# Kernel tuning notes

Hardware: AMD Instinct MI355X
Metric: run time of the kernel (lower is better)

The kernel has to match this reference:

```python
import jax, jax.numpy as jnp
import numpy as np

D_MODEL = 1024
NUM_HEADS = 16
HEAD_DIM = D_MODEL // NUM_HEADS


def setup_inputs() -> dict:
    key = jax.random.key(0)
    ks = jax.random.split(key, 9)
    s = 1.0 / np.sqrt(D_MODEL)  # torch Linear default init range scale
    def lin(k):
        kw, kb = jax.random.split(k)
        W = jax.random.uniform(kw, (D_MODEL, D_MODEL), jnp.float32, -s, s)
        b = jax.random.uniform(kb, (D_MODEL,), jnp.float32, -s, s)
        return W, b
    Wq, bq = lin(ks[0])
    Wk, bk = lin(ks[1])
    Wv, bv = lin(ks[2])
    Wo, bo = lin(ks[3])
    x = jax.random.normal(ks[4], (4, 2048, D_MODEL), jnp.float32)
    return {"x": x, "Wq": Wq, "bq": bq, "Wk": Wk, "bk": bk,
            "Wv": Wv, "bv": bv, "Wo": Wo, "bo": bo}


def reference(x, Wq, bq, Wk, bk, Wv, bv, Wo, bo):
    B, S, _ = x.shape
    H, Dh = NUM_HEADS, HEAD_DIM
    scale = Dh ** -0.5
    # projections; W stored as [in, out] so y = x @ W + b
    q = (x @ Wq + bq).reshape(B, S, H, Dh).transpose(0, 2, 1, 3)  # [B,H,S,Dh]
    k = (x @ Wk + bk).reshape(B, S, H, Dh).transpose(0, 2, 1, 3)
    v = (x @ Wv + bv).reshape(B, S, H, Dh).transpose(0, 2, 1, 3)
    scores = jnp.einsum('bhqd,bhkd->bhqk', q, k) * scale  # [B,H,S,S]
    causal = jnp.tril(jnp.ones((S, S), dtype=bool))
    scores = jnp.where(causal[None, None], scores, jnp.finfo(scores.dtype).min)
    attn = jax.nn.softmax(scores, axis=-1)
    out = jnp.einsum('bhqk,bhkd->bhqd', attn, v)  # [B,H,S,Dh]
    out = out.transpose(0, 2, 1, 3).reshape(B, S, H * Dh)
    return out @ Wo + bo
```

## Files before the change

kernel.cpp:

```cpp
#include <hip/hip_runtime.h>
#include <math.h>

#define DM 1024
#define NH 16
#define DH 64
#define BB 4
#define SS 2048
#define MROWS (BB*SS)

typedef __bf16 bf16;
typedef __bf16 bf16x2 __attribute__((ext_vector_type(2)));
typedef __bf16 bf16x8 __attribute__((ext_vector_type(8)));
typedef float floatx4 __attribute__((ext_vector_type(4)));
typedef unsigned int uintx4 __attribute__((ext_vector_type(4)));
typedef unsigned int uintx2 __attribute__((ext_vector_type(2)));

#if __has_builtin(__builtin_amdgcn_exp2f)
#define EXP2F __builtin_amdgcn_exp2f
#else
#define EXP2F exp2f
#endif

#define QSCALE (0.125f * 1.44269504088896f)

__device__ __forceinline__ void cp16(void* lds, const void* g) {
  __builtin_amdgcn_global_load_lds(
      (__attribute__((address_space(1))) void*)(void*)g,
      (__attribute__((address_space(3))) void*)lds,
      16, 0, 0);
}

__device__ __forceinline__ unsigned pk2(float a, float b) {
  bf16x2 t;
  t[0] = (bf16)a;
  t[1] = (bf16)b;
  return __builtin_bit_cast(unsigned, t);
}

#if __has_builtin(__builtin_amdgcn_permlane32_swap) && \
    __has_builtin(__builtin_amdgcn_permlane16_swap)
__device__ __forceinline__ void pl32(unsigned& a, unsigned& b) {
  uintx2 r = __builtin_amdgcn_permlane32_swap(a, b, false, false);
  a = r[0]; b = r[1];
}
__device__ __forceinline__ void pl16(unsigned& a, unsigned& b) {
  uintx2 r = __builtin_amdgcn_permlane16_swap(a, b, false, false);
  a = r[0]; b = r[1];
}
#else
__device__ __forceinline__ void pl32(unsigned& a, unsigned& b) {
  asm volatile("v_permlane32_swap_b32 %0, %1" : "+v"(a), "+v"(b));
}
__device__ __forceinline__ void pl16(unsigned& a, unsigned& b) {
  asm volatile("v_permlane16_swap_b32 %0, %1" : "+v"(a), "+v"(b));
}
#endif

__global__ __launch_bounds__(256) void cvt_x(
    const float* __restrict__ X, bf16* __restrict__ Y) {
  int i = (blockIdx.x * 256 + threadIdx.x) * 8;
  float4 a = *(const float4*)&X[i];
  float4 b = *(const float4*)&X[i + 4];
  bf16x8 o;
  o[0] = (bf16)a.x; o[1] = (bf16)a.y; o[2] = (bf16)a.z; o[3] = (bf16)a.w;
  o[4] = (bf16)b.x; o[5] = (bf16)b.y; o[6] = (bf16)b.z; o[7] = (bf16)b.w;
  *(bf16x8*)&Y[i] = o;
}

__global__ __launch_bounds__(1024) void wtransc(
    const float* __restrict__ W0, const float* __restrict__ W1,
    const float* __restrict__ W2, const float* __restrict__ W3,
    bf16* __restrict__ T0, bf16* __restrict__ T1,
    bf16* __restrict__ T2, bf16* __restrict__ T3) {
  __shared__ float tile[32][33];
  const float* W; bf16* T;
  int z = blockIdx.z;
  if (z == 0)      { W = W0; T = T0; }
  else if (z == 1) { W = W1; T = T1; }
  else if (z == 2) { W = W2; T = T2; }
  else             { W = W3; T = T3; }
  int tx = threadIdx.x, ty = threadIdx.y;
  tile[ty][tx] = W[(blockIdx.y * 32 + ty) * DM + blockIdx.x * 32 + tx];
  __syncthreads();
  T[(blockIdx.x * 32 + ty) * DM + blockIdx.y * 32 + tx] = (bf16)tile[tx][ty];
}

#define BK 32
#define TST 136

__global__ __launch_bounds__(256, 3) void gemm_qkv(
    const bf16* __restrict__ A, const bf16* __restrict__ WT,
    const float* __restrict__ bq, const float* __restrict__ bk,
    const float* __restrict__ bv,
    bf16* __restrict__ qb, bf16* __restrict__ kb, bf16* __restrict__ vt) {
  __shared__ __align__(16) char smem[2 * 128 * BK * 2 * 2 > 128 * TST * 2
                                         ? 2 * 128 * BK * 2 * 2
                                         : 128 * TST * 2];
  bf16* As = (bf16*)smem;
  bf16* Bs = (bf16*)smem + 2 * 128 * BK;
  bf16* Ts = (bf16*)smem;

  int tid = threadIdx.x;
  int lane = tid & 63, w = tid >> 6;
  int wm = (w >> 1) * 64;
  int wn = (w & 1) * 64;
  int m0 = blockIdx.y * 128;
  int n0 = blockIdx.x * 128;
  int which = n0 >> 10;
  int qd = lane >> 4;
  int l15 = lane & 15;

  floatx4 acc[4][4] = {};

  auto stage = [&](int pb, int k0) {
    for (int i = 0; i < 2; ++i) {
      int ci = (w * 2 + i) * 64;
      int c = ci + lane;
      int r = c >> 2, cc = (c & 3) * 8;
      cp16(&As[pb * 128 * BK + ci * 8], &A[(size_t)(m0 + r) * DM + k0 + cc]);
      cp16(&Bs[pb * 128 * BK + ci * 8], &WT[(size_t)(n0 + r) * DM + k0 + cc]);
    }
  };

  stage(0, 0);
  __syncthreads();

  for (int t = 0; t < DM / BK; ++t) {
    int pb = t & 1;
    if (t + 1 < DM / BK) stage(pb ^ 1, (t + 1) * BK);
    bf16x8 af[4], bfr[4];
    for (int mt = 0; mt < 4; ++mt)
      af[mt] = *(const bf16x8*)&As[pb * 128 * BK + (wm + mt * 16 + l15) * BK + qd * 8];
    for (int nt = 0; nt < 4; ++nt)
      bfr[nt] = *(const bf16x8*)&Bs[pb * 128 * BK + (wn + nt * 16 + l15) * BK + qd * 8];
    for (int mt = 0; mt < 4; ++mt)
      for (int nt = 0; nt < 4; ++nt)
        acc[mt][nt] = __builtin_amdgcn_mfma_f32_16x16x32_bf16(
            af[mt], bfr[nt], acc[mt][nt], 0, 0, 0);
    __syncthreads();
  }

  const float* bias = (which == 0) ? bq : (which == 1) ? bk : bv;

  if (which == 2) {
    for (int nt = 0; nt < 4; ++nt) {
      int cl = wn + nt * 16 + l15;
      float bv_ = bias[(n0 & 1023) + cl];
      for (int mt = 0; mt < 4; ++mt)
        for (int r = 0; r < 4; ++r)
          Ts[cl * TST + wm + mt * 16 + qd * 4 + r] = (bf16)(acc[mt][nt][r] + bv_);
    }
    __syncthreads();
    int chunk = tid & 15, colb = tid >> 4;
    for (int p = 0; p < 8; ++p) {
      int cl = p * 16 + colb;
      bf16x8 vv = *(const bf16x8*)&Ts[cl * TST + chunk * 8];
      *(bf16x8*)&vt[(size_t)((n0 & 1023) + cl) * MROWS + m0 + chunk * 8] = vv;
    }
  } else {
    bf16* out = (which == 0) ? qb : kb;
    float sc = (which == 0) ? QSCALE : 1.0f;
    for (int nt = 0; nt < 4; ++nt) {
      int col = (n0 & 1023) + wn + nt * 16 + l15;
      float bv_ = bias[col];
      for (int mt = 0; mt < 4; ++mt)
        for (int r = 0; r < 4; ++r) {
          int row = m0 + wm + mt * 16 + qd * 4 + r;
          out[(size_t)row * DM + col] = (bf16)((acc[mt][nt][r] + bv_) * sc);
        }
    }
  }
}

__global__ __launch_bounds__(256, 4) void gemm_out(
    const bf16* __restrict__ A, const bf16* __restrict__ WT,
    const float* __restrict__ bias, float* __restrict__ C) {
  __shared__ __align__(16) bf16 As[2][64 * BK];
  __shared__ __align__(16) bf16 Bs[2][128 * BK];
  int tid = threadIdx.x;
  int lane = tid & 63, w = tid >> 6;
  int wm = (w >> 1) * 32;
  int wn = (w & 1) * 64;
  int m0 = blockIdx.x * 64;
  int n0 = blockIdx.y * 128;
  int qd = lane >> 4;
  int l15 = lane & 15;

  floatx4 acc[2][4] = {};

  auto stage = [&](int pb, int k0) {
    {
      int ci = w * 64;
      int c = ci + lane;
      int r = c >> 2, cc = (c & 3) * 8;
      cp16(&As[pb][ci * 8], &A[(size_t)(m0 + r) * DM + k0 + cc]);
    }
    for (int i = 0; i < 2; ++i) {
      int ci = (w * 2 + i) * 64;
      int c = ci + lane;
      int r = c >> 2, cc = (c & 3) * 8;
      cp16(&Bs[pb][ci * 8], &WT[(size_t)(n0 + r) * DM + k0 + cc]);
    }
  };

  stage(0, 0);
  __syncthreads();

  for (int t = 0; t < DM / BK; ++t) {
    int pb = t & 1;
    if (t + 1 < DM / BK) stage(pb ^ 1, (t + 1) * BK);
    bf16x8 af[2], bfr[4];
    for (int mt = 0; mt < 2; ++mt)
      af[mt] = *(const bf16x8*)&As[pb][(wm + mt * 16 + l15) * BK + qd * 8];
    for (int nt = 0; nt < 4; ++nt)
      bfr[nt] = *(const bf16x8*)&Bs[pb][(wn + nt * 16 + l15) * BK + qd * 8];
    for (int mt = 0; mt < 2; ++mt)
      for (int nt = 0; nt < 4; ++nt)
        acc[mt][nt] = __builtin_amdgcn_mfma_f32_16x16x32_bf16(
            af[mt], bfr[nt], acc[mt][nt], 0, 0, 0);
    __syncthreads();
  }

  for (int nt = 0; nt < 4; ++nt) {
    int col = n0 + wn + nt * 16 + l15;
    float bv = bias[col];
    for (int mt = 0; mt < 2; ++mt)
      for (int r = 0; r < 4; ++r) {
        int row = m0 + wm + mt * 16 + qd * 4 + r;
        C[(size_t)row * DM + col] = acc[mt][nt][r] + bv;
      }
  }
}

__global__ __launch_bounds__(512, 4) void attn_fwd(
    const bf16* __restrict__ Qg, const bf16* __restrict__ Kg,
    const bf16* __restrict__ Vt, bf16* __restrict__ O) {
  __shared__ __align__(16) bf16 Kbuf[2][64 * 64];
  __shared__ __align__(16) bf16 Vbuf[2][64 * 64];

  int tid = threadIdx.x;
  int lane = tid & 63, w = tid >> 6;
  int qd = lane >> 4, l15 = lane & 15;
  int sw = l15 & 7;
  int pair = blockIdx.x, h = blockIdx.y, b = blockIdx.z;
  int base = b * SS;
  int hoff = h * DH;

  int gch = ((lane & 7) ^ (lane >> 3)) * 8;
  auto stage = [&](int pb, int kt) {
    int kbase = base + kt * 64;
    int ci = w * 64;
    int row = (ci + lane) >> 3;
    cp16(&Kbuf[pb][ci * 8], &Kg[(size_t)(kbase + row) * DM + hoff + gch]);
    cp16(&Vbuf[pb][ci * 8],
         &Vt[(size_t)(hoff + row) * MROWS + base + kt * 64 + gch]);
  };

  for (int ph = 0; ph < 2; ++ph) {
    int qt = ph ? (15 - pair) : pair;
    int q0 = qt * 128;
    int nkt = 2 * qt + 2;

    stage(0, 0);

    bf16x8 qf[2];
    {
      int qrow = base + q0 + w * 16 + l15;
      for (int ks = 0; ks < 2; ++ks)
        qf[ks] = *(const bf16x8*)&Qg[(size_t)qrow * DM + hoff + ks * 32 + qd * 8];
    }

    float m_r = -3e38f;
    float lacc = 0.0f;
    floatx4 oacc[4] = {};

    __syncthreads();

    for (int kt = 0; kt < nkt; ++kt) {
      int pb = kt & 1;
      if (kt + 1 < nkt) stage(pb ^ 1, kt + 1);

      floatx4 s[4] = {};
      for (int ks = 0; ks < 2; ++ks)
        for (int nt = 0; nt < 4; ++nt) {
          bf16x8 kf = *(const bf16x8*)
              &Kbuf[pb][(nt * 16 + l15) * 64 + (((ks << 2) + qd) ^ sw) * 8];
          s[nt] = __builtin_amdgcn_mfma_f32_16x16x32_bf16(
              kf, qf[ks], s[nt], 0, 0, 0);
        }

      int rowq = q0 + w * 16 + l15;
      if (kt >= 2 * qt) {
        for (int nt = 0; nt < 4; ++nt)
          for (int r = 0; r < 4; ++r) {
            int col = kt * 64 + nt * 16 + qd * 4 + r;
            if (col > rowq) s[nt][r] = -3e38f;
          }
      }

      floatx4 m4 = s[0];
      for (int nt = 1; nt < 4; ++nt)
        for (int r = 0; r < 4; ++r) m4[r] = fmaxf(m4[r], s[nt][r]);
      float t = fmaxf(fmaxf(m4[0], m4[1]), fmaxf(m4[2], m4[3]));
      t = fmaxf(t, __shfl_xor(t, 16, 64));
      t = fmaxf(t, __shfl_xor(t, 32, 64));

      if (!__all(t <= m_r + 11.0f)) {
        float mn = fmaxf(m_r, t);
        float al = EXP2F(m_r - mn);
        m_r = mn;
        for (int dt = 0; dt < 4; ++dt)
          for (int r = 0; r < 4; ++r) oacc[dt][r] *= al;
        lacc *= al;
      }

      bf16x8 pf[2];
      for (int ks = 0; ks < 2; ++ks) {
        float pu[4], pv[4];
        for (int r = 0; r < 4; ++r) {
          pu[r] = EXP2F(s[2 * ks][r] - m_r);
          pv[r] = EXP2F(s[2 * ks + 1][r] - m_r);
        }
        lacc += ((pu[0] + pu[1]) + (pu[2] + pu[3])) +
                ((pv[0] + pv[1]) + (pv[2] + pv[3]));
        unsigned u0 = pk2(pu[0], pu[1]), u1 = pk2(pu[2], pu[3]);
        unsigned v0 = pk2(pv[0], pv[1]), v1 = pk2(pv[2], pv[3]);
        pl32(u0, v0); pl16(u0, v0);
        pl32(u1, v1); pl16(u1, v1);
        uintx4 ww;
        ww[0] = u0; ww[1] = u1; ww[2] = v0; ww[3] = v1;
        pf[ks] = __builtin_bit_cast(bf16x8, ww);
      }

      for (int ks = 0; ks < 2; ++ks)
        for (int dt = 0; dt < 4; ++dt) {
          bf16x8 vf = *(const bf16x8*)
              &Vbuf[pb][(dt * 16 + l15) * 64 + (((ks << 2) + qd) ^ sw) * 8];
          oacc[dt] = __builtin_amdgcn_mfma_f32_16x16x32_bf16(
              pf[ks], vf, oacc[dt], 0, 0, 0);
        }

      __syncthreads();
    }

    lacc += __shfl_xor(lacc, 16, 64);
    lacc += __shfl_xor(lacc, 32, 64);
    for (int r = 0; r < 4; ++r) {
      float inv = 1.0f / __shfl(lacc, qd * 4 + r, 64);
      int row = base + q0 + w * 16 + qd * 4 + r;
      for (int dt = 0; dt < 4; ++dt)
        O[(size_t)row * DM + hoff + dt * 16 + l15] = (bf16)(oacc[dt][r] * inv);
    }
  }
}

extern "C" void kernel_launch(void* const* d_in, const int* in_sizes, int n_in,
                              void* d_out, int out_size, void* d_ws, size_t ws_size,
                              hipStream_t stream) {
  const float* x  = (const float*)d_in[0];
  const float* Wq = (const float*)d_in[1];
  const float* bq = (const float*)d_in[2];
  const float* Wk = (const float*)d_in[3];
  const float* bk = (const float*)d_in[4];
  const float* Wv = (const float*)d_in[5];
  const float* bv = (const float*)d_in[6];
  const float* Wo = (const float*)d_in[7];
  const float* bo = (const float*)d_in[8];
  float* out = (float*)d_out;

  char* ws = (char*)d_ws;
  const size_t act = (size_t)MROWS * DM * sizeof(bf16);
  bf16* xb    = (bf16*)(ws);
  bf16* qb    = (bf16*)(ws + act);
  bf16* kb    = (bf16*)(ws + 2 * act);
  bf16* vt    = (bf16*)(ws + 3 * act);
  bf16* ab    = (bf16*)(ws + 4 * act);
  bf16* WqkvT = (bf16*)(ws + 5 * act);
  bf16* WoT   = WqkvT + 3 * (size_t)DM * DM;

  cvt_x<<<MROWS * DM / (256 * 8), 256, 0, stream>>>(x, xb);
  wtransc<<<dim3(32, 32, 4), dim3(32, 32), 0, stream>>>(
      Wq, Wk, Wv, Wo,
      WqkvT, WqkvT + (size_t)DM * DM, WqkvT + 2 * (size_t)DM * DM, WoT);

  gemm_qkv<<<dim3(24, 64), 256, 0, stream>>>(
      xb, WqkvT, bq, bk, bv, qb, kb, vt);

  attn_fwd<<<dim3(8, NH, BB), 512, 0, stream>>>(qb, kb, vt, ab);

  gemm_out<<<dim3(128, 8), 256, 0, stream>>>(ab, WoT, bo, out);
}
```

Measured before the change: 258.7 us.

## Restructure QKV GEMM into 256x128 tiles with swizzled LDS and staged pipeline

Rewrites the fused QKV projection GEMM to use 512-thread blocks computing 256x128 output tiles with a K-step of 64. Shared memory uses an XOR swizzle so fragment reads avoid bank conflicts. The A and B loads are split into staggered stages overlapped with two MFMA phases, using explicit waitcnt, barriers and setprio. A block-index remap groups tiles for better L2 reuse. The larger tile cuts global traffic per FLOP, but it uses much more LDS and allows only one block per CU, and the hand-written waitcnt ordering is fragile.

```diff
diff --git a/kernel.cpp b/kernel.cpp
--- a/kernel.cpp
+++ b/kernel.cpp
@@ -86,86 +86,134 @@
 }
 
 #define BK 32
-#define TST 136
-
-__global__ __launch_bounds__(256, 3) void gemm_qkv(
+
+__global__ __launch_bounds__(512, 1) void gemm_qkv(
     const bf16* __restrict__ A, const bf16* __restrict__ WT,
     const float* __restrict__ bq, const float* __restrict__ bk,
     const float* __restrict__ bv,
     bf16* __restrict__ qb, bf16* __restrict__ kb, bf16* __restrict__ vt) {
-  __shared__ __align__(16) char smem[2 * 128 * BK * 2 * 2 > 128 * TST * 2
-                                         ? 2 * 128 * BK * 2 * 2
-                                         : 128 * TST * 2];
-  bf16* As = (bf16*)smem;
-  bf16* Bs = (bf16*)smem + 2 * 128 * BK;
+  __shared__ __align__(16) char smem[(2 * 256 * 64 + 2 * 128 * 64) * 2];
+  bf16* Ab = (bf16*)smem;
+  bf16* Bb = (bf16*)(smem + 2 * 256 * 64 * 2);
   bf16* Ts = (bf16*)smem;
 
   int tid = threadIdx.x;
   int lane = tid & 63, w = tid >> 6;
-  int wm = (w >> 1) * 64;
-  int wn = (w & 1) * 64;
-  int m0 = blockIdx.y * 128;
-  int n0 = blockIdx.x * 128;
+  int wr = w >> 1, wc = w & 1;
+  int qd = lane >> 4, l15 = lane & 15;
+
+  int bid = blockIdx.x;
+  int wg = (bid & 7) * 96 + (bid >> 3);
+  int mb = wg / 24, nb = wg % 24;
+  int m0 = mb * 256;
+  int n0 = nb * 128;
   int which = n0 >> 10;
-  int qd = lane >> 4;
-  int l15 = lane & 15;
 
   floatx4 acc[4][4] = {};
 
-  auto stage = [&](int pb, int k0) {
+  auto stageA = [&](int pb, int t, int hf) {
     for (int i = 0; i < 2; ++i) {
-      int ci = (w * 2 + i) * 64;
-      int c = ci + lane;
-      int r = c >> 2, cc = (c & 3) * 8;
-      cp16(&As[pb * 128 * BK + ci * 8], &A[(size_t)(m0 + r) * DM + k0 + cc]);
-      cp16(&Bs[pb * 128 * BK + ci * 8], &WT[(size_t)(n0 + r) * DM + k0 + cc]);
-    }
-  };
-
-  stage(0, 0);
+      int L = i * 512 + tid;
+      int row = L >> 3, ch = L & 7;
+      int sch = ch ^ (row & 7);
+      cp16(&Ab[pb * 256 * 64 + (hf * 128 + row) * 64 + ch * 8],
+           &A[(size_t)(m0 + hf * 128 + row) * DM + t * 64 + sch * 8]);
+    }
+  };
+  auto stageB = [&](int pb, int t) {
+    for (int i = 0; i < 2; ++i) {
+      int L = i * 512 + tid;
+      int row = L >> 3, ch = L & 7;
+      int sch = ch ^ (row & 7);
+      cp16(&Bb[pb * 128 * 64 + row * 64 + ch * 8],
+           &WT[(size_t)(n0 + row) * DM + t * 64 + sch * 8]);
+    }
+  };
+  auto ldA = [&](int pb, int mt, int ks) -> bf16x8 {
+    int row = wr * 64 + mt * 16 + l15;
+    int c = ((ks << 2) + qd) ^ (row & 7);
+    return *(const bf16x8*)&Ab[pb * 256 * 64 + row * 64 + c * 8];
+  };
+  auto ldB = [&](int pb, int nt, int ks) -> bf16x8 {
+    int row = wc * 64 + nt * 16 + l15;
+    int c = ((ks << 2) + qd) ^ (row & 7);
+    return *(const bf16x8*)&Bb[pb * 128 * 64 + row * 64 + c * 8];
+  };
+
+  stageA(0, 0, 0);
+  stageA(0, 0, 1);
+  stageB(0, 0);
+  stageB(1, 1);
+  asm volatile("s_waitcnt vmcnt(2)" ::: "memory");
+  __builtin_amdgcn_s_barrier();
+
+  for (int g = 0; g < 16; ++g) {
+    int pb = g & 1;
+    bf16x8 af0[2][2], bfr[4][2];
+    for (int mt = 0; mt < 2; ++mt)
+      for (int ks = 0; ks < 2; ++ks) af0[mt][ks] = ldA(pb, mt, ks);
+    for (int nt = 0; nt < 4; ++nt)
+      for (int ks = 0; ks < 2; ++ks) bfr[nt][ks] = ldB(pb, nt, ks);
+    if (g + 1 < 16) { stageA(pb ^ 1, g + 1, 0); stageA(pb ^ 1, g + 1, 1); }
+    __builtin_amdgcn_s_barrier();
+    asm volatile("s_waitcnt lgkmcnt(0)" ::: "memory");
+    __builtin_amdgcn_sched_barrier(0);
+    __builtin_amdgcn_s_setprio(1);
+    for (int mt = 0; mt < 2; ++mt)
+      for (int nt = 0; nt < 4; ++nt)
+        for (int ks = 0; ks < 2; ++ks)
+          acc[mt][nt] = __builtin_amdgcn_mfma_f32_16x16x32_bf16(
+              af0[mt][ks], bfr[nt][ks], acc[mt][nt], 0, 0, 0);
+    __builtin_amdgcn_s_setprio(0);
+    __builtin_amdgcn_s_barrier();
+    bf16x8 af1[2][2];
+    for (int mt = 0; mt < 2; ++mt)
+      for (int ks = 0; ks < 2; ++ks) af1[mt][ks] = ldA(pb, 2 + mt, ks);
+    if (g + 2 < 16) stageB(pb, g + 2);
+    __builtin_amdgcn_s_barrier();
+    asm volatile("s_waitcnt lgkmcnt(0)" ::: "memory");
+    __builtin_amdgcn_sched_barrier(0);
+    __builtin_amdgcn_s_setprio(1);
+    for (int mt = 0; mt < 2; ++mt)
+      for (int nt = 0; nt < 4; ++nt)
+        for (int ks = 0; ks < 2; ++ks)
+          acc[2 + mt][nt] = __builtin_amdgcn_mfma_f32_16x16x32_bf16(
+              af1[mt][ks], bfr[nt][ks], acc[2 + mt][nt], 0, 0, 0);
+    __builtin_amdgcn_s_setprio(0);
+    if (g < 14)
+      asm volatile("s_waitcnt vmcnt(2)" ::: "memory");
+    else if (g == 14)
+      asm volatile("s_waitcnt vmcnt(0)" ::: "memory");
+    __builtin_amdgcn_s_barrier();
+  }
+
   __syncthreads();
-
-  for (int t = 0; t < DM / BK; ++t) {
-    int pb = t & 1;
-    if (t + 1 < DM / BK) stage(pb ^ 1, (t + 1) * BK);
-    bf16x8 af[4], bfr[4];
-    for (int mt = 0; mt < 4; ++mt)
-      af[mt] = *(const bf16x8*)&As[pb * 128 * BK + (wm + mt * 16 + l15) * BK + qd * 8];
-    for (int nt = 0; nt < 4; ++nt)
-      bfr[nt] = *(const bf16x8*)&Bs[pb * 128 * BK + (wn + nt * 16 + l15) * BK + qd * 8];
-    for (int mt = 0; mt < 4; ++mt)
-      for (int nt = 0; nt < 4; ++nt)
-        acc[mt][nt] = __builtin_amdgcn_mfma_f32_16x16x32_bf16(
-            af[mt], bfr[nt], acc[mt][nt], 0, 0, 0);
-    __syncthreads();
-  }
 
   const float* bias = (which == 0) ? bq : (which == 1) ? bk : bv;
 
   if (which == 2) {
     for (int nt = 0; nt < 4; ++nt) {
-      int cl = wn + nt * 16 + l15;
-      float bv_ = bias[(n0 & 1023) + cl];
+      int dl = wc * 64 + nt * 16 + l15;
+      float bv_ = bias[(n0 & 1023) + dl];
       for (int mt = 0; mt < 4; ++mt)
         for (int r = 0; r < 4; ++r)
-          Ts[cl * TST + wm + mt * 16 + qd * 4 + r] = (bf16)(acc[mt][nt][r] + bv_);
+          Ts[dl * 264 + wr * 64 + mt * 16 + qd * 4 + r] =
+              (bf16)(acc[mt][nt][r] + bv_);
     }
     __syncthreads();
-    int chunk = tid & 15, colb = tid >> 4;
-    for (int p = 0; p < 8; ++p) {
-      int cl = p * 16 + colb;
-      bf16x8 vv = *(const bf16x8*)&Ts[cl * TST + chunk * 8];
-      *(bf16x8*)&vt[(size_t)((n0 & 1023) + cl) * MROWS + m0 + chunk * 8] = vv;
-    }
+    int dl = tid >> 2, s0 = (tid & 3) * 64;
+    size_t vrow = (size_t)((n0 & 1023) + dl) * MROWS + m0 + s0;
+    for (int j = 0; j < 8; ++j)
+      *(bf16x8*)&vt[vrow + j * 8] = *(const bf16x8*)&Ts[dl * 264 + s0 + j * 8];
   } else {
     bf16* out = (which == 0) ? qb : kb;
     float sc = (which == 0) ? QSCALE : 1.0f;
     for (int nt = 0; nt < 4; ++nt) {
-      int col = (n0 & 1023) + wn + nt * 16 + l15;
+      int col = (n0 & 1023) + wc * 64 + nt * 16 + l15;
       float bv_ = bias[col];
       for (int mt = 0; mt < 4; ++mt)
         for (int r = 0; r < 4; ++r) {
-          int row = m0 + wm + mt * 16 + qd * 4 + r;
+          int row = m0 + wr * 64 + mt * 16 + qd * 4 + r;
           out[(size_t)row * DM + col] = (bf16)((acc[mt][nt][r] + bv_) * sc);
         }
     }
@@ -383,7 +431,7 @@
       Wq, Wk, Wv, Wo,
       WqkvT, WqkvT + (size_t)DM * DM, WqkvT + 2 * (size_t)DM * DM, WoT);
 
-  gemm_qkv<<<dim3(24, 64), 256, 0, stream>>>(
+  gemm_qkv<<<768, 512, 0, stream>>>(
       xb, WqkvT, bq, bk, bv, qb, kb, vt);
 
   attn_fwd<<<dim3(8, NH, BB), 512, 0, stream>>>(qb, kb, vt, ab);
```

Result: slower. 263.8 us (+2.0%).
